# Kernel optimization log

Hardware: AMD Instinct MI355X
Metric: run time of the kernel (lower is better)

## Reference

```python
import jax, jax.numpy as jnp
import numpy as np

T, L, C = 128, 32, 4
B, D = 32, 512


def _compute_content_matrix(T, L, C):
    # Precomputed sparse weighting tensor: for each (window start i, window end j),
    # C clip-averaging rows over the frames covered by that window.
    Wc = np.zeros((L, L, C, T), dtype=np.float32)
    for i in range(L):
        for j in range(i, L):
            window_size = j - i + 1
            window_start, num_frames = i * (T // L), window_size * (T // L)
            clip_size = max(1, num_frames // C)
            for c in range(min(C, num_frames)):
                s = window_start + c * clip_size
                Wc[i, j, c, s:s + clip_size] = 1.0 / clip_size
    return Wc


def setup_inputs() -> dict:
    key = jax.random.key(0)
    k1, k2 = jax.random.split(key)
    f = jax.random.normal(k1, (B, T, D), dtype=jnp.float32)
    moment_mask = jax.random.uniform(k2, (B, L, L), dtype=jnp.float32)
    Wc = jnp.asarray(_compute_content_matrix(T, L, C))
    return {"f": f, "moment_mask": moment_mask, "Wc": Wc}


def reference(f, moment_mask, Wc):
    # fc: [B, L, L, C, D] -- clip features per (start,end) window, masked
    fc = jnp.einsum('lmct,btd->blmcd', Wc, f) * moment_mask[:, :, :, None, None]
    # fm: [B, L, L, D] -- mean over clips
    fm = jnp.mean(fc, axis=3)
    # fb: [B, L, D] -- boundary features = non-overlapping avg pool of size T//L
    b, t, d = f.shape
    l = Wc.shape[0]
    fb = f.reshape(b, l, t // l, d).mean(axis=2)
    return (fc, fm, fb)
```

## Files before the change

### kernel.cpp

```cpp
#include <hip/hip_runtime.h>

#define TT 128
#define LL 32
#define CC 4
#define BB 32
#define DD 512
#define D4 (DD / 4)

__device__ __forceinline__ float4 diff_scale(float4 a, float4 b, float s) {
    return make_float4((a.x - b.x) * s, (a.y - b.y) * s,
                       (a.z - b.z) * s, (a.w - b.w) * s);
}

__global__ __launch_bounds__(64) void prefix_kernel(const float4* __restrict__ f4,
                                                    float4* __restrict__ P4) {
    int idx = blockIdx.x * 64 + threadIdx.x;
    int b = idx >> 7;
    int d4 = idx & (D4 - 1);
    const float4* fp = f4 + (size_t)b * TT * D4 + d4;
    float4* Pp = P4 + (size_t)b * (TT + 1) * D4 + d4;
    float4 acc = make_float4(0.f, 0.f, 0.f, 0.f);
    Pp[0] = acc;
#pragma unroll 16
    for (int t = 0; t < TT; ++t) {
        float4 v = fp[(size_t)t * D4];
        acc.x += v.x; acc.y += v.y; acc.z += v.z; acc.w += v.w;
        Pp[(size_t)(t + 1) * D4] = acc;
    }
}

__global__ __launch_bounds__(128) void fused_kernel(const float4* __restrict__ P4,
                                                    const float* __restrict__ mask,
                                                    float4* __restrict__ fc4,
                                                    float4* __restrict__ fm4,
                                                    float4* __restrict__ fb4) {
    int h = blockIdx.x;
    int logical = ((h & 7) << 7) | (h >> 3);
    int b = logical >> 5;
    int i = logical & (LL - 1);
    int tid = threadIdx.x;

    const float4* Pb = P4 + (size_t)b * (TT + 1) * D4 + tid;
    size_t base = ((size_t)b * LL + i) * LL;
    float4* fcb = fc4 + base * CC * D4 + tid;
    float4* fmb = fm4 + base * D4 + tid;
    const float* mrow = mask + base;

    float4 z = make_float4(0.f, 0.f, 0.f, 0.f);
    for (int j = 0; j < i; ++j) {
        float4* o = fcb + (size_t)j * CC * D4;
        o[0] = z; o[D4] = z; o[2 * D4] = z; o[3 * D4] = z;
        fmb[(size_t)j * D4] = z;
    }

    int s0 = 4 * i;
    float4 p0 = Pb[(size_t)s0 * D4];

    {
        float4 q = Pb[(size_t)(s0 + 4) * D4];
        fb4[((size_t)b * LL + i) * D4 + tid] = diff_scale(q, p0, 0.25f);
    }

    for (int j = i; j < LL; ++j) {
        int ws = j - i + 1;
        float4 p1 = Pb[(size_t)(s0 + ws) * D4];
        float4 p2 = Pb[(size_t)(s0 + 2 * ws) * D4];
        float4 p3 = Pb[(size_t)(s0 + 3 * ws) * D4];
        float4 p4 = Pb[(size_t)(s0 + 4 * ws) * D4];
        float sc = mrow[j] / (float)ws;
        float sm = 0.25f * sc;
        float4* o = fcb + (size_t)j * CC * D4;
        o[0]      = diff_scale(p1, p0, sc);
        o[D4]     = diff_scale(p2, p1, sc);
        o[2 * D4] = diff_scale(p3, p2, sc);
        o[3 * D4] = diff_scale(p4, p3, sc);
        fmb[(size_t)j * D4] = diff_scale(p4, p0, sm);
    }
}

__global__ __launch_bounds__(256) void fcfm_direct(const float* __restrict__ f,
                                                   const float* __restrict__ mask,
                                                   float* __restrict__ fc,
                                                   float* __restrict__ fm) {
    int blk = blockIdx.x;
    int j = blk & (LL - 1);
    int i = (blk >> 5) & (LL - 1);
    int b = blk >> 10;
    int tid = threadIdx.x;
    float* fc_out = fc + (size_t)blk * CC * DD;
    float* fm_out = fm + (size_t)blk * DD;

    if (j < i) {
        float4 z = make_float4(0.f, 0.f, 0.f, 0.f);
        float4* fcv = (float4*)fc_out;
#pragma unroll
        for (int k = 0; k < 2; ++k) fcv[tid + k * 256] = z;
        float4* fmv = (float4*)fm_out;
        if (tid < DD / 4) fmv[tid] = z;
        return;
    }

    int ws = j - i + 1;
    float sc = mask[blk] / (float)ws;
    const float* fbase = f + (size_t)b * TT * DD;

#pragma unroll
    for (int r = 0; r < 2; ++r) {
        int dd = tid + r * 256;
        float tot = 0.f;
#pragma unroll
        for (int c = 0; c < CC; ++c) {
            float s = 0.f;
            int t0 = 4 * i + c * ws;
            for (int t = 0; t < ws; ++t) s += fbase[(size_t)(t0 + t) * DD + dd];
            fc_out[c * DD + dd] = s * sc;
            tot += s;
        }
        fm_out[dd] = tot * sc * 0.25f;
    }
}

__global__ __launch_bounds__(256) void fb_direct(const float* __restrict__ f,
                                                 float* __restrict__ fb) {
    int idx = blockIdx.x * 256 + threadIdx.x;
    int d = idx & (DD - 1);
    int l = (idx >> 9) & (LL - 1);
    int b = idx >> 14;
    const float* fp = f + (size_t)b * TT * DD + d;
    int t0 = 4 * l;
    fb[idx] = (fp[(size_t)t0 * DD] + fp[(size_t)(t0 + 1) * DD] +
               fp[(size_t)(t0 + 2) * DD] + fp[(size_t)(t0 + 3) * DD]) * 0.25f;
}

extern "C" void kernel_launch(void* const* d_in, const int* in_sizes, int n_in,
                              void* d_out, int out_size, void* d_ws, size_t ws_size,
                              hipStream_t stream) {
    const float* f    = (const float*)d_in[0];
    const float* mask = (const float*)d_in[1];

    float* out = (float*)d_out;
    const size_t fc_elems = (size_t)BB * LL * LL * CC * DD;
    const size_t fm_elems = (size_t)BB * LL * LL * DD;
    float* fc = out;
    float* fm = out + fc_elems;
    float* fb = out + fc_elems + fm_elems;

    const size_t P_bytes = (size_t)BB * (TT + 1) * DD * sizeof(float);

    if (ws_size >= P_bytes) {
        float* P = (float*)d_ws;
        prefix_kernel<<<(BB * D4) / 64, 64, 0, stream>>>((const float4*)f,
                                                         (float4*)P);
        fused_kernel<<<BB * LL, 128, 0, stream>>>((const float4*)P, mask,
                                                  (float4*)fc, (float4*)fm,
                                                  (float4*)fb);
    } else {
        fcfm_direct<<<BB * LL * LL, 256, 0, stream>>>(f, mask, fc, fm);
        fb_direct<<<(BB * LL * DD) / 256, 256, 0, stream>>>(f, fb);
    }
}
```

Measured before the change: 409.1 us.

## Split fused kernel to one block per (b,i,j) window with nontemporal stores

Replaces the per-(b,i) block that loops over all j with one block per (b,i,j) output window, raising the grid from 1024 to 32768 blocks and balancing the triangular workload. Output writes use nontemporal stores so the large fc/fm streams bypass cache. The fb output is produced by the j==i block. The cost is more block launch overhead and redundant reloads of the p0 prefix row per window.

```diff
diff --git a/kernel.cpp b/kernel.cpp
--- a/kernel.cpp
+++ b/kernel.cpp
@@ -7,74 +7,77 @@
 #define DD 512
 #define D4 (DD / 4)
 
-__device__ __forceinline__ float4 diff_scale(float4 a, float4 b, float s) {
-    return make_float4((a.x - b.x) * s, (a.y - b.y) * s,
-                       (a.z - b.z) * s, (a.w - b.w) * s);
+typedef float fx4 __attribute__((ext_vector_type(4)));
+
+__device__ __forceinline__ void nt_store(fx4 v, const fx4* p) {
+    __builtin_nontemporal_store(v, (fx4*)p);
 }
 
-__global__ __launch_bounds__(64) void prefix_kernel(const float4* __restrict__ f4,
-                                                    float4* __restrict__ P4) {
+__device__ __forceinline__ fx4 diff_scale(fx4 a, fx4 b, float s) {
+    return (a - b) * s;
+}
+
+__global__ __launch_bounds__(64) void prefix_kernel(const fx4* __restrict__ f4,
+                                                    fx4* __restrict__ P4) {
     int idx = blockIdx.x * 64 + threadIdx.x;
     int b = idx >> 7;
     int d4 = idx & (D4 - 1);
-    const float4* fp = f4 + (size_t)b * TT * D4 + d4;
-    float4* Pp = P4 + (size_t)b * (TT + 1) * D4 + d4;
-    float4 acc = make_float4(0.f, 0.f, 0.f, 0.f);
+    const fx4* fp = f4 + (size_t)b * TT * D4 + d4;
+    fx4* Pp = P4 + (size_t)b * (TT + 1) * D4 + d4;
+    fx4 acc = (fx4)0.f;
     Pp[0] = acc;
 #pragma unroll 16
     for (int t = 0; t < TT; ++t) {
-        float4 v = fp[(size_t)t * D4];
-        acc.x += v.x; acc.y += v.y; acc.z += v.z; acc.w += v.w;
+        acc += fp[(size_t)t * D4];
         Pp[(size_t)(t + 1) * D4] = acc;
     }
 }
 
-__global__ __launch_bounds__(128) void fused_kernel(const float4* __restrict__ P4,
-                                                    const float* __restrict__ mask,
-                                                    float4* __restrict__ fc4,
-                                                    float4* __restrict__ fm4,
-                                                    float4* __restrict__ fb4) {
+__global__ __launch_bounds__(128) void fcfm_kernel(const fx4* __restrict__ P4,
+                                                   const float* __restrict__ mask,
+                                                   fx4* __restrict__ fc4,
+                                                   fx4* __restrict__ fm4,
+                                                   fx4* __restrict__ fb4) {
     int h = blockIdx.x;
-    int logical = ((h & 7) << 7) | (h >> 3);
-    int b = logical >> 5;
-    int i = logical & (LL - 1);
+    int blk = ((h & 7) << 12) | (h >> 3);
+    int j = blk & (LL - 1);
+    int i = (blk >> 5) & (LL - 1);
+    int b = blk >> 10;
     int tid = threadIdx.x;
+    fx4* fc_out = fc4 + (size_t)blk * CC * D4 + tid;
+    fx4* fm_out = fm4 + (size_t)blk * D4 + tid;
 
-    const float4* Pb = P4 + (size_t)b * (TT + 1) * D4 + tid;
-    size_t base = ((size_t)b * LL + i) * LL;
-    float4* fcb = fc4 + base * CC * D4 + tid;
-    float4* fmb = fm4 + base * D4 + tid;
-    const float* mrow = mask + base;
-
-    float4 z = make_float4(0.f, 0.f, 0.f, 0.f);
-    for (int j = 0; j < i; ++j) {
-        float4* o = fcb + (size_t)j * CC * D4;
-        o[0] = z; o[D4] = z; o[2 * D4] = z; o[3 * D4] = z;
-        fmb[(size_t)j * D4] = z;
+    if (j < i) {
+        fx4 z = (fx4)0.f;
+        nt_store(z, fc_out);
+        nt_store(z, fc_out + D4);
+        nt_store(z, fc_out + 2 * D4);
+        nt_store(z, fc_out + 3 * D4);
+        nt_store(z, fm_out);
+        return;
     }
 
+    int ws = j - i + 1;
+    float sc = mask[blk] / (float)ws;
+    float sm = 0.25f * sc;
+    const fx4* Pb = P4 + (size_t)b * (TT + 1) * D4 + tid;
     int s0 = 4 * i;
-    float4 p0 = Pb[(size_t)s0 * D4];
 
-    {
-        float4 q = Pb[(size_t)(s0 + 4) * D4];
-        fb4[((size_t)b * LL + i) * D4 + tid] = diff_scale(q, p0, 0.25f);
-    }
+    fx4 p0 = Pb[(size_t)(s0) * D4];
+    fx4 p1 = Pb[(size_t)(s0 + ws) * D4];
+    fx4 p2 = Pb[(size_t)(s0 + 2 * ws) * D4];
+    fx4 p3 = Pb[(size_t)(s0 + 3 * ws) * D4];
+    fx4 p4 = Pb[(size_t)(s0 + 4 * ws) * D4];
 
-    for (int j = i; j < LL; ++j) {
-        int ws = j - i + 1;
-        float4 p1 = Pb[(size_t)(s0 + ws) * D4];
-        float4 p2 = Pb[(size_t)(s0 + 2 * ws) * D4];
-        float4 p3 = Pb[(size_t)(s0 + 3 * ws) * D4];
-        float4 p4 = Pb[(size_t)(s0 + 4 * ws) * D4];
-        float sc = mrow[j] / (float)ws;
-        float sm = 0.25f * sc;
-        float4* o = fcb + (size_t)j * CC * D4;
-        o[0]      = diff_scale(p1, p0, sc);
-        o[D4]     = diff_scale(p2, p1, sc);
-        o[2 * D4] = diff_scale(p3, p2, sc);
-        o[3 * D4] = diff_scale(p4, p3, sc);
-        fmb[(size_t)j * D4] = diff_scale(p4, p0, sm);
+    nt_store(diff_scale(p1, p0, sc), fc_out);
+    nt_store(diff_scale(p2, p1, sc), fc_out + D4);
+    nt_store(diff_scale(p3, p2, sc), fc_out + 2 * D4);
+    nt_store(diff_scale(p4, p3, sc), fc_out + 3 * D4);
+    nt_store(diff_scale(p4, p0, sm), fm_out);
+
+    if (j == i) {
+        nt_store(diff_scale(p4, p0, 0.25f),
+                 fb4 + ((size_t)b * LL + i) * D4 + tid);
     }
 }
 
@@ -91,11 +94,11 @@
     float* fm_out = fm + (size_t)blk * DD;
 
     if (j < i) {
-        float4 z = make_float4(0.f, 0.f, 0.f, 0.f);
-        float4* fcv = (float4*)fc_out;
+        fx4 z = (fx4)0.f;
+        fx4* fcv = (fx4*)fc_out;
 #pragma unroll
         for (int k = 0; k < 2; ++k) fcv[tid + k * 256] = z;
-        float4* fmv = (float4*)fm_out;
+        fx4* fmv = (fx4*)fm_out;
         if (tid < DD / 4) fmv[tid] = z;
         return;
     }
@@ -149,11 +152,11 @@
 
     if (ws_size >= P_bytes) {
         float* P = (float*)d_ws;
-        prefix_kernel<<<(BB * D4) / 64, 64, 0, stream>>>((const float4*)f,
-                                                         (float4*)P);
-        fused_kernel<<<BB * LL, 128, 0, stream>>>((const float4*)P, mask,
-                                                  (float4*)fc, (float4*)fm,
-                                                  (float4*)fb);
+        prefix_kernel<<<(BB * D4) / 64, 64, 0, stream>>>((const fx4*)f,
+                                                         (fx4*)P);
+        fcfm_kernel<<<BB * LL * LL, 128, 0, stream>>>((const fx4*)P, mask,
+                                                      (fx4*)fc, (fx4*)fm,
+                                                      (fx4*)fb);
     } else {
         fcfm_direct<<<BB * LL * LL, 256, 0, stream>>>(f, mask, fc, fm);
         fb_direct<<<(BB * LL * DD) / 256, 256, 0, stream>>>(f, fb);
```

Result: faster. 356.4 us (-12.9%).
